# Performance work log

Hardware: AMD Instinct MI355X
Metric: run time of the kernel (lower is better)

Reference implementation:

```python
import jax, jax.numpy as jnp
import numpy as np
import math

B, S, HID = 2, 2048, 1024
NH = 16
HD = HID // NH  # 64
CHUNK = 128  # min(128, S) from the module


def setup_inputs() -> dict:
    key = jax.random.key(0)
    ks = jax.random.split(key, 8)
    scale = 1.0 / math.sqrt(HID)
    return {
        "hidden_states": jax.random.normal(ks[0], (B, S, HID), jnp.float32),
        "attention_mask": jnp.zeros((B, S, S), jnp.float32),
        "Wq": jax.random.normal(ks[1], (HID, HID), jnp.float32) * scale,
        "bq": jnp.zeros((HID,), jnp.float32),
        "Wk": jax.random.normal(ks[2], (HID, HID), jnp.float32) * scale,
        "bk": jnp.zeros((HID,), jnp.float32),
        "Wv": jax.random.normal(ks[3], (HID, HID), jnp.float32) * scale,
        "bv": jnp.zeros((HID,), jnp.float32),
        "head_weights": jnp.ones((NH,), jnp.float32),
    }


def _split_heads(x):
    # [B,S,HID] -> [B,NH,S,HD]
    b, s, _ = x.shape
    return x.reshape(b, s, NH, HD).transpose(0, 2, 1, 3)


def reference(hidden_states, attention_mask, Wq, bq, Wk, bk, Wv, bv, head_weights):
    # nn.Linear: y = x @ W.T + b
    q = _split_heads(hidden_states @ Wq.T + bq)  # [B,NH,S,HD]
    k = _split_heads(hidden_states @ Wk.T + bk)
    v = _split_heads(hidden_states @ Wv.T + bv)

    scores = jnp.einsum("bhqd,bhkd->bhqk", q, k) / math.sqrt(HD)
    scores = scores + attention_mask[:, None, :, :]  # additive mask broadcast over heads
    probs = jax.nn.softmax(scores, axis=-1)
    # dropout p=0.0 -> identity; post-softmax head-weight scaling (head_pruning)
    probs = probs * head_weights[None, :, None, None]
    ctx = jnp.einsum("bhqk,bhkd->bhqd", probs, v)  # [B,NH,S,HD]
    context_layer = ctx.transpose(0, 2, 1, 3).reshape(B, S, HID)

    # module returns the probs of the LAST query chunk of the python loop
    last_start = ((S + CHUNK - 1) // CHUNK - 1) * CHUNK
    output_attention_probs = probs[:, :, last_start:S, :]  # [B,NH,128,S]
    return context_layer, output_attention_probs
```

## Files before the change

### kernel.cpp

```cpp
#include <hip/hip_runtime.h>

typedef unsigned short u16;
typedef __attribute__((ext_vector_type(8))) short bf16x8;
typedef __attribute__((ext_vector_type(4))) float f32x4;

#define B_   2
#define S_   2048
#define HID_ 1024
#define NH_  16
#define HD_  64
#define SCALE_ 0.125f

__device__ __forceinline__ u16 f2bf(float f) {
    union { float f; unsigned int i; } v; v.f = f;
    unsigned int r = v.i + 0x7fffu + ((v.i >> 16) & 1u);
    return (u16)(r >> 16);
}
__device__ __forceinline__ bf16x8 ld8(const u16* p) {
    return *reinterpret_cast<const bf16x8*>(p);
}
__device__ __forceinline__ unsigned cvtpk(float lo, float hi) {
    unsigned r;
    asm("v_cvt_pk_bf16_f32 %0, %1, %2" : "=v"(r) : "v"(lo), "v"(hi));
    return r;
}
__device__ __forceinline__ void gll16(const u16* g, const u16* l) {
    __builtin_amdgcn_global_load_lds(
        (const __attribute__((address_space(1))) unsigned int*)g,
        (__attribute__((address_space(3))) unsigned int*)l, 16, 0, 0);
}

__global__ __launch_bounds__(256) void convert_bf16(
    const float* __restrict__ X, const float* __restrict__ W0,
    const float* __restrict__ W1, const float* __restrict__ W2,
    u16* __restrict__ Xb, u16* __restrict__ Wb)
{
    const size_t s = (size_t)blockIdx.x * 256 + threadIdx.x;
    const float* src; u16* dst; size_t off;
    if (s < 524288) { src = X; dst = Xb; off = s * 8; }
    else {
        const size_t t = s - 524288;
        const int w = (int)(t >> 17);
        off = (t & 131071) * 8;
        src = w == 0 ? W0 : w == 1 ? W1 : W2;
        dst = Wb + (size_t)w * 1048576;
    }
    f32x4 a = *(const f32x4*)(src + off);
    f32x4 b = *(const f32x4*)(src + off + 4);
    bf16x8 r;
    #pragma unroll
    for (int e = 0; e < 4; e++) { r[e] = (short)f2bf(a[e]); r[4 + e] = (short)f2bf(b[e]); }
    *(bf16x8*)(dst + off) = r;
}

__global__ __launch_bounds__(256) void mask_scan(
    const unsigned* __restrict__ m, unsigned* __restrict__ flag)
{
    const size_t i = ((size_t)blockIdx.x * 256 + threadIdx.x) * 8;
    const uint4* p = (const uint4*)(m + i);
    uint4 a = p[0], b = p[1];
    const unsigned M = 0x7fffffffu;
    unsigned v = (a.x & M) | (a.y & M) | (a.z & M) | (a.w & M)
               | (b.x & M) | (b.y & M) | (b.z & M) | (b.w & M);
    if (v) atomicOr(flag, 1u);
}

#define BK_ 32

__global__ __launch_bounds__(256) void qkv_mfma(
    const u16* __restrict__ Xb, const u16* __restrict__ Wb,
    const float* __restrict__ bq, const float* __restrict__ bk,
    const float* __restrict__ bv,
    u16* __restrict__ Q, u16* __restrict__ K, u16* __restrict__ V)
{
    __shared__ __align__(16) u16 As[128 * BK_];
    __shared__ __align__(16) u16 Bs[128 * BK_];

    const int tid  = threadIdx.x;
    const int wave = tid >> 6;
    const int lane = tid & 63;
    const int l16  = lane & 15;
    const int quad = lane >> 4;
    const int wr   = wave >> 1, wc = wave & 1;

    const int i0 = blockIdx.x * 128;
    const int j0 = blockIdx.y * 128;

    const int grow = (wave * 64 + lane) >> 2;
    const int gcol = (lane & 3) * 8;
    const u16* ldsA0 = As + wave * 512;
    const u16* ldsA1 = As + 2048 + wave * 512;
    const u16* ldsB0 = Bs + wave * 512;
    const u16* ldsB1 = Bs + 2048 + wave * 512;

    f32x4 acc[4][4] = {};

    for (int k0 = 0; k0 < HID_; k0 += BK_) {
        __syncthreads();
        gll16(Xb + (size_t)(i0 + grow) * HID_ + k0 + gcol, ldsA0);
        gll16(Xb + (size_t)(i0 + 64 + grow) * HID_ + k0 + gcol, ldsA1);
        gll16(Wb + (size_t)(j0 + grow) * HID_ + k0 + gcol, ldsB0);
        gll16(Wb + (size_t)(j0 + 64 + grow) * HID_ + k0 + gcol, ldsB1);
        __syncthreads();

        bf16x8 af[4], bfr[4];
        #pragma unroll
        for (int mt = 0; mt < 4; mt++)
            af[mt] = ld8(&As[(wr * 64 + mt * 16 + l16) * BK_ + quad * 8]);
        #pragma unroll
        for (int nt = 0; nt < 4; nt++)
            bfr[nt] = ld8(&Bs[(wc * 64 + nt * 16 + l16) * BK_ + quad * 8]);
        #pragma unroll
        for (int mt = 0; mt < 4; mt++)
            #pragma unroll
            for (int nt = 0; nt < 4; nt++)
                acc[mt][nt] = __builtin_amdgcn_mfma_f32_16x16x32_bf16(af[mt], bfr[nt], acc[mt][nt], 0, 0, 0);
    }

    const int which = j0 >> 10;
    const float* bias = which == 0 ? bq : which == 1 ? bk : bv;
    u16* Y            = which == 0 ? Q  : which == 1 ? K  : V;

    u16* bb = (wave < 2) ? (As + wave * 2048) : (Bs + (wave - 2) * 2048);

    #pragma unroll
    for (int p = 0; p < 2; p++) {
        __syncthreads();
        #pragma unroll
        for (int t2 = 0; t2 < 2; t2++) {
            const int nt = 2 * p + t2;
            const int j  = j0 + wc * 64 + nt * 16 + l16;
            const int jj = j & 1023;
            const float bv_ = bias[jj];
            #pragma unroll
            for (int mt = 0; mt < 4; mt++)
                #pragma unroll
                for (int r = 0; r < 4; r++) {
                    const int row = mt * 16 + quad * 4 + r;
                    const int col = t2 * 16 + l16;
                    const u16 val = f2bf(acc[mt][nt][r] + bv_);
                    if (which == 2)
                        bb[col * 64 + (row ^ ((col & 7) << 3))] = val;
                    else
                        bb[row * 32 + (col ^ ((row & 0xC) << 1))] = val;
                }
        }
        __syncthreads();
        #pragma unroll
        for (int k = 0; k < 4; k++) {
            const int c = lane + 64 * k;
            if (which == 2) {
                const int col  = c >> 3;
                const int row0 = (c & 7) * 8;
                bf16x8 v = ld8(&bb[col * 64 + (row0 ^ ((col & 7) << 3))]);
                const int j  = j0 + wc * 64 + p * 32 + col;
                const int jj = j & 1023;
                const int h = jj >> 6, d = jj & 63;
                const int i = i0 + wr * 64 + row0;
                const int b = i >> 11, s = i & (S_ - 1);
                *(bf16x8*)&Y[((size_t)(b * NH_ + h) * HD_ + d) * S_ + s] = v;
            } else {
                const int row  = c >> 2;
                const int col0 = (c & 3) * 8;
                bf16x8 v = ld8(&bb[row * 32 + (col0 ^ ((row & 0xC) << 1))]);
                const int j  = j0 + wc * 64 + p * 32 + col0;
                const int jj = j & 1023;
                const int h = jj >> 6, d = jj & 63;
                const int i = i0 + wr * 64 + row;
                const int b = i >> 11, s = i & (S_ - 1);
                *(bf16x8*)&Y[(((size_t)(b * NH_ + h) * S_ + s) * HD_) + d] = v;
            }
        }
    }
}

__global__ __launch_bounds__(256) void attn(
    const u16* __restrict__ Q, const u16* __restrict__ K, const u16* __restrict__ Vt,
    const float* __restrict__ mask, const float* __restrict__ hw,
    const unsigned* __restrict__ mflag,
    float* __restrict__ ctx, float* __restrict__ ml)
{
    __shared__ __align__(16) u16 Ks[2][64 * 64];
    __shared__ __align__(16) u16 Vs[2][64 * 64];
    __shared__ __align__(16) u16 Pl[4][16 * 64];

    const int usemask = (mflag[0] != 0);

    const int tid  = threadIdx.x;
    const int wave = tid >> 6;
    const int lane = tid & 63;
    const int l16  = lane & 15;
    const int quad = lane >> 4;
    const int x7   = l16 & 7;

    const int lin = blockIdx.x + 32 * (blockIdx.y + 16 * blockIdx.z);
    const int xcd = lin & 7, jj = lin >> 3;
    const int qb  = jj & 31;
    const int hb  = xcd * 4 + (jj >> 5);
    const int h   = hb & 15, b = hb >> 4;
    const int bh  = b * NH_ + h;

    const u16* Qh  = Q  + (size_t)bh * S_ * HD_;
    const u16* Kh  = K  + (size_t)bh * S_ * HD_;
    const u16* Vth = Vt + (size_t)bh * HD_ * S_;
    const float* Mb = mask + (size_t)b * S_ * S_;

    const int q0 = qb * 64 + wave * 16;

    bf16x8 qf0 = ld8(Qh + (size_t)(q0 + l16) * HD_ + quad * 8);
    bf16x8 qf1 = ld8(Qh + (size_t)(q0 + l16) * HD_ + 32 + quad * 8);

    f32x4 oacc[4] = {};
    float l_part[4] = {0.f, 0.f, 0.f, 0.f};

    const int srow = tid >> 3;
    const int sch  = tid & 7;
    const int ssw  = (sch ^ (srow & 7)) * 8;
    const int sL   = srow * 64 + ssw;

    {
        bf16x8 k0 = ld8(Kh + (size_t)srow * HD_ + sch * 8);
        bf16x8 k1 = ld8(Kh + (size_t)(srow + 32) * HD_ + sch * 8);
        bf16x8 v0 = ld8(Vth + (size_t)srow * S_ + sch * 8);
        bf16x8 v1 = ld8(Vth + (size_t)(srow + 32) * S_ + sch * 8);
        *(bf16x8*)&Ks[0][sL] = k0; *(bf16x8*)&Ks[0][sL + 2048] = k1;
        *(bf16x8*)&Vs[0][sL] = v0; *(bf16x8*)&Vs[0][sL + 2048] = v1;
    }
    __syncthreads();

    for (int t = 0; t < 32; ++t) {
        const int cur = t & 1;
        const int kt  = t * 64;
        const u16* Kb = Ks[cur];
        const u16* Vb = Vs[cur];

        bf16x8 kr0, kr1, vr0, vr1;
        if (t < 31) {
            const u16* Kg = Kh + (size_t)(kt + 64) * HD_;
            kr0 = ld8(Kg + (size_t)srow * HD_ + sch * 8);
            kr1 = ld8(Kg + (size_t)(srow + 32) * HD_ + sch * 8);
            vr0 = ld8(Vth + (size_t)srow * S_ + kt + 64 + sch * 8);
            vr1 = ld8(Vth + (size_t)(srow + 32) * S_ + kt + 64 + sch * 8);
        }

        f32x4 sacc[4] = {};
        __builtin_amdgcn_s_setprio(1);
        #pragma unroll
        for (int nb = 0; nb < 4; nb++) {
            const int base = (nb * 16 + l16) * 64;
            bf16x8 k0 = ld8(&Kb[base + ((quad ^ x7) * 8)]);
            bf16x8 k1 = ld8(&Kb[base + (((quad + 4) ^ x7) * 8)]);
            sacc[nb] = __builtin_amdgcn_mfma_f32_16x16x32_bf16(qf0, k0, sacc[nb], 0, 0, 0);
            sacc[nb] = __builtin_amdgcn_mfma_f32_16x16x32_bf16(qf1, k1, sacc[nb], 0, 0, 0);
        }
        __builtin_amdgcn_s_setprio(0);

        float p[4][4];
        if (usemask) {
            #pragma unroll
            for (int nb = 0; nb < 4; nb++)
                #pragma unroll
                for (int r = 0; r < 4; r++) {
                    const int qrow = q0 + quad * 4 + r;
                    const int key  = kt + nb * 16 + l16;
                    float s = sacc[nb][r] * SCALE_ + Mb[(size_t)qrow * S_ + key];
                    p[nb][r] = __expf(fminf(s, 80.f));
                    l_part[r] += p[nb][r];
                }
        } else {
            #pragma unroll
            for (int nb = 0; nb < 4; nb++)
                #pragma unroll
                for (int r = 0; r < 4; r++) {
                    p[nb][r] = __expf(fminf(sacc[nb][r] * SCALE_, 80.f));
                    l_part[r] += p[nb][r];
                }
        }

        {
            char* pbase = (char*)&Pl[wave][0];
            const int r0 = quad * 4;
            #pragma unroll
            for (int nb = 0; nb < 4; nb++) {
                const unsigned w01 = cvtpk(p[nb][0], p[nb][1]);
                const unsigned w23 = cvtpk(p[nb][2], p[nb][3]);
                const int c0 = nb * 32 + l16 * 2;
                *(u16*)(pbase + (r0 + 0) * 128 + (c0 ^ (((r0 + 0) & 7) << 4))) = (u16)w01;
                *(u16*)(pbase + (r0 + 1) * 128 + (c0 ^ (((r0 + 1) & 7) << 4))) = (u16)(w01 >> 16);
                *(u16*)(pbase + (r0 + 2) * 128 + (c0 ^ (((r0 + 2) & 7) << 4))) = (u16)w23;
                *(u16*)(pbase + (r0 + 3) * 128 + (c0 ^ (((r0 + 3) & 7) << 4))) = (u16)(w23 >> 16);
            }
        }

        __builtin_amdgcn_s_setprio(1);
        #pragma unroll
        for (int kb = 0; kb < 2; kb++) {
            const int c = kb * 4 + quad;
            bf16x8 pf = ld8(&Pl[wave][l16 * 64 + ((c ^ x7) * 8)]);
            #pragma unroll
            for (int db = 0; db < 4; db++) {
                bf16x8 vf = ld8(&Vb[(db * 16 + l16) * 64 + ((c ^ x7) * 8)]);
                oacc[db] = __builtin_amdgcn_mfma_f32_16x16x32_bf16(pf, vf, oacc[db], 0, 0, 0);
            }
        }
        __builtin_amdgcn_s_setprio(0);

        if (t < 31) {
            u16* Kd = Ks[cur ^ 1]; u16* Vd = Vs[cur ^ 1];
            *(bf16x8*)&Kd[sL] = kr0; *(bf16x8*)&Kd[sL + 2048] = kr1;
            *(bf16x8*)&Vd[sL] = vr0; *(bf16x8*)&Vd[sL + 2048] = vr1;
        }
        __syncthreads();
    }

    float l_i[4];
    #pragma unroll
    for (int r = 0; r < 4; r++) {
        float s = l_part[r];
        #pragma unroll
        for (int off = 1; off < 16; off <<= 1) s += __shfl_xor(s, off);
        l_i[r] = s;
    }

    const float hwf = hw[h];
    float invl[4];
    #pragma unroll
    for (int r = 0; r < 4; r++) invl[r] = hwf / l_i[r];

    #pragma unroll
    for (int db = 0; db < 4; db++)
        #pragma unroll
        for (int r = 0; r < 4; r++) {
            const int qrow = q0 + quad * 4 + r;
            ctx[((size_t)(b * S_ + qrow)) * HID_ + h * HD_ + db * 16 + l16] =
                oacc[db][r] * invl[r];
        }

    if (qb >= 30 && l16 == 0) {
        #pragma unroll
        for (int r = 0; r < 4; r++) {
            const int qrow = q0 + quad * 4 + r;
            ml[bh * 128 + (qrow - 1920)] = l_i[r];
        }
    }
}

__global__ __launch_bounds__(256) void probs_qk(
    const u16* __restrict__ Q, const u16* __restrict__ K,
    const float* __restrict__ mask, const float* __restrict__ hw,
    const unsigned* __restrict__ mflag, const float* __restrict__ ml,
    float* __restrict__ probs_out)
{
    const int usemask = (mflag[0] != 0);

    const int tid  = threadIdx.x;
    const int wave = tid >> 6;
    const int lane = tid & 63;
    const int l16  = lane & 15;
    const int quad = lane >> 4;

    const int rt = blockIdx.x & 1;
    const int ks = blockIdx.x >> 1;
    const int h  = blockIdx.y;
    const int b  = blockIdx.z;
    const int bh = b * NH_ + h;

    const u16* Qh = Q + (size_t)bh * S_ * HD_;
    const u16* Kh = K + (size_t)bh * S_ * HD_;
    const float* Mb = mask + (size_t)b * S_ * S_;

    const int q0 = 1920 + rt * 64 + wave * 16;

    bf16x8 qf0 = ld8(Qh + (size_t)(q0 + l16) * HD_ + quad * 8);
    bf16x8 qf1 = ld8(Qh + (size_t)(q0 + l16) * HD_ + 32 + quad * 8);

    const float hwf = hw[h];
    float invl[4];
    #pragma unroll
    for (int r = 0; r < 4; r++)
        invl[r] = hwf / ml[bh * 128 + (q0 - 1920) + quad * 4 + r];

    for (int kt = ks * 512; kt < ks * 512 + 512; kt += 64) {
        f32x4 sacc[4] = {};
        #pragma unroll
        for (int nb = 0; nb < 4; nb++) {
            const u16* krow = Kh + (size_t)(kt + nb * 16 + l16) * HD_ + quad * 8;
            bf16x8 k0 = ld8(krow);
            bf16x8 k1 = ld8(krow + 32);
            sacc[nb] = __builtin_amdgcn_mfma_f32_16x16x32_bf16(qf0, k0, sacc[nb], 0, 0, 0);
            sacc[nb] = __builtin_amdgcn_mfma_f32_16x16x32_bf16(qf1, k1, sacc[nb], 0, 0, 0);
        }
        #pragma unroll
        for (int nb = 0; nb < 4; nb++)
            #pragma unroll
            for (int r = 0; r < 4; r++) {
                const int qrow = q0 + quad * 4 + r;
                const int key  = kt + nb * 16 + l16;
                float s = sacc[nb][r] * SCALE_;
                if (usemask) s += Mb[(size_t)qrow * S_ + key];
                probs_out[((size_t)bh * 128 + (qrow - 1920)) * S_ + key] =
                    __expf(fminf(s, 80.f)) * invl[r];
            }
    }
}

extern "C" void kernel_launch(void* const* d_in, const int* in_sizes, int n_in,
                              void* d_out, int out_size, void* d_ws, size_t ws_size,
                              hipStream_t stream)
{
    const void* X = 0; const void* mask = 0; const void* hw = 0;
    const void* Wm[3] = {0, 0, 0}; const void* bm[3] = {0, 0, 0};
    int wi = 0, bi = 0;
    for (int i = 0; i < n_in; i++) {
        switch (in_sizes[i]) {
            case 4194304: X = d_in[i]; break;
            case 8388608: mask = d_in[i]; break;
            case 1048576: if (wi < 3) Wm[wi++] = d_in[i]; break;
            case 1024:    if (bi < 3) bm[bi++] = d_in[i]; break;
            case 16:      hw = d_in[i]; break;
            default: break;
        }
    }
    if (!X || !mask || wi != 3 || bi != 3 || !hw) {
        X = d_in[0]; mask = d_in[1];
        Wm[0] = d_in[2]; bm[0] = d_in[3];
        Wm[1] = d_in[4]; bm[1] = d_in[5];
        Wm[2] = d_in[6]; bm[2] = d_in[7];
        hw = d_in[8];
    }

    u16* Q  = (u16*)d_ws;
    u16* Kw = Q + 4194304ull;
    u16* Vw = Kw + 4194304ull;
    u16* Xb = Vw + 4194304ull;
    u16* Wb = Xb + 4194304ull;
    unsigned* flag = (unsigned*)(Wb + 3145728ull);
    float* ml = (float*)(flag + 64);

    float* ctx   = (float*)d_out;
    float* probs = ctx + (size_t)B_ * S_ * HID_;

    hipMemsetAsync(flag, 0, 4, stream);
    mask_scan<<<4096, 256, 0, stream>>>((const unsigned*)mask, flag);
    convert_bf16<<<3584, 256, 0, stream>>>(
        (const float*)X, (const float*)Wm[0], (const float*)Wm[1], (const float*)Wm[2],
        Xb, Wb);

    qkv_mfma<<<dim3(32, 24), dim3(256), 0, stream>>>(
        Xb, Wb, (const float*)bm[0], (const float*)bm[1], (const float*)bm[2],
        Q, Kw, Vw);

    attn<<<dim3(32, 16, 2), dim3(256), 0, stream>>>(
        Q, Kw, Vw, (const float*)mask, (const float*)hw, flag, ctx, ml);

    probs_qk<<<dim3(8, 16, 2), dim3(256), 0, stream>>>(
        Q, Kw, (const float*)mask, (const float*)hw, flag, ml, probs);
}
```

Measured before the change: 248.8 us.

## Fuse convert and mask-scan kernels, XCD-aware GEMM tiling, vectorized probs writes

```diff
diff --git a/kernel.cpp b/kernel.cpp
--- a/kernel.cpp
+++ b/kernel.cpp
@@ -30,39 +30,39 @@
         (__attribute__((address_space(3))) unsigned int*)l, 16, 0, 0);
 }
 
-__global__ __launch_bounds__(256) void convert_bf16(
+__global__ __launch_bounds__(256) void conv_scan(
     const float* __restrict__ X, const float* __restrict__ W0,
     const float* __restrict__ W1, const float* __restrict__ W2,
-    u16* __restrict__ Xb, u16* __restrict__ Wb)
+    const unsigned* __restrict__ m,
+    u16* __restrict__ Xb, u16* __restrict__ Wb, unsigned* __restrict__ flag)
 {
-    const size_t s = (size_t)blockIdx.x * 256 + threadIdx.x;
-    const float* src; u16* dst; size_t off;
-    if (s < 524288) { src = X; dst = Xb; off = s * 8; }
-    else {
-        const size_t t = s - 524288;
-        const int w = (int)(t >> 17);
-        off = (t & 131071) * 8;
-        src = w == 0 ? W0 : w == 1 ? W1 : W2;
-        dst = Wb + (size_t)w * 1048576;
-    }
-    f32x4 a = *(const f32x4*)(src + off);
-    f32x4 b = *(const f32x4*)(src + off + 4);
-    bf16x8 r;
-    #pragma unroll
-    for (int e = 0; e < 4; e++) { r[e] = (short)f2bf(a[e]); r[4 + e] = (short)f2bf(b[e]); }
-    *(bf16x8*)(dst + off) = r;
-}
-
-__global__ __launch_bounds__(256) void mask_scan(
-    const unsigned* __restrict__ m, unsigned* __restrict__ flag)
-{
-    const size_t i = ((size_t)blockIdx.x * 256 + threadIdx.x) * 8;
-    const uint4* p = (const uint4*)(m + i);
-    uint4 a = p[0], b = p[1];
-    const unsigned M = 0x7fffffffu;
-    unsigned v = (a.x & M) | (a.y & M) | (a.z & M) | (a.w & M)
-               | (b.x & M) | (b.y & M) | (b.z & M) | (b.w & M);
-    if (v) atomicOr(flag, 1u);
+    const int bx = blockIdx.x;
+    if (bx < 3584) {
+        const size_t s = (size_t)bx * 256 + threadIdx.x;
+        const float* src; u16* dst; size_t off;
+        if (s < 524288) { src = X; dst = Xb; off = s * 8; }
+        else {
+            const size_t t = s - 524288;
+            const int w = (int)(t >> 17);
+            off = (t & 131071) * 8;
+            src = w == 0 ? W0 : w == 1 ? W1 : W2;
+            dst = Wb + (size_t)w * 1048576;
+        }
+        f32x4 a = *(const f32x4*)(src + off);
+        f32x4 b = *(const f32x4*)(src + off + 4);
+        bf16x8 r;
+        #pragma unroll
+        for (int e = 0; e < 4; e++) { r[e] = (short)f2bf(a[e]); r[4 + e] = (short)f2bf(b[e]); }
+        *(bf16x8*)(dst + off) = r;
+    } else {
+        const size_t i = ((size_t)(bx - 3584) * 256 + threadIdx.x) * 8;
+        const uint4* p = (const uint4*)(m + i);
+        uint4 a = p[0], b = p[1];
+        const unsigned M = 0x7fffffffu;
+        unsigned v = (a.x & M) | (a.y & M) | (a.z & M) | (a.w & M)
+                   | (b.x & M) | (b.y & M) | (b.z & M) | (b.w & M);
+        if (v) atomicOr(flag, 1u);
+    }
 }
 
 #define BK_ 32
@@ -83,8 +83,11 @@
     const int quad = lane >> 4;
     const int wr   = wave >> 1, wc = wave & 1;
 
-    const int i0 = blockIdx.x * 128;
-    const int j0 = blockIdx.y * 128;
+    const int id  = blockIdx.x + 32 * blockIdx.y;
+    const int xcd = id & 7;
+    const int kk  = id >> 3;
+    const int i0  = (xcd * 4 + (kk & 3)) * 128;
+    const int j0  = (kk >> 2) * 128;
 
     const int grow = (wave * 64 + lane) >> 2;
     const int gcol = (lane & 3) * 8;
@@ -369,38 +372,44 @@
     const u16* Kh = K + (size_t)bh * S_ * HD_;
     const float* Mb = mask + (size_t)b * S_ * S_;
 
-    const int q0 = 1920 + rt * 64 + wave * 16;
-
-    bf16x8 qf0 = ld8(Qh + (size_t)(q0 + l16) * HD_ + quad * 8);
-    bf16x8 qf1 = ld8(Qh + (size_t)(q0 + l16) * HD_ + 32 + quad * 8);
-
-    const float hwf = hw[h];
-    float invl[4];
-    #pragma unroll
-    for (int r = 0; r < 4; r++)
-        invl[r] = hwf / ml[bh * 128 + (q0 - 1920) + quad * 4 + r];
-
-    for (int kt = ks * 512; kt < ks * 512 + 512; kt += 64) {
+    const int q0   = 1920 + rt * 64 + wave * 16;
+    const int qrow = q0 + l16;
+
+    bf16x8 qf0 = ld8(Qh + (size_t)qrow * HD_ + quad * 8);
+    bf16x8 qf1 = ld8(Qh + (size_t)qrow * HD_ + 32 + quad * 8);
+
+    const float invl = hw[h] / ml[bh * 128 + (qrow - 1920)];
+    float* Prow = probs_out + ((size_t)bh * 128 + (qrow - 1920)) * S_;
+    const float* Mrow = Mb + (size_t)qrow * S_;
+
+    for (int kt = ks * 256; kt < ks * 256 + 256; kt += 64) {
         f32x4 sacc[4] = {};
         #pragma unroll
         for (int nb = 0; nb < 4; nb++) {
             const u16* krow = Kh + (size_t)(kt + nb * 16 + l16) * HD_ + quad * 8;
-            bf16x8 k0 = ld8(krow);
-            bf16x8 k1 = ld8(krow + 32);
-            sacc[nb] = __builtin_amdgcn_mfma_f32_16x16x32_bf16(qf0, k0, sacc[nb], 0, 0, 0);
-            sacc[nb] = __builtin_amdgcn_mfma_f32_16x16x32_bf16(qf1, k1, sacc[nb], 0, 0, 0);
-        }
-        #pragma unroll
-        for (int nb = 0; nb < 4; nb++)
-            #pragma unroll
-            for (int r = 0; r < 4; r++) {
-                const int qrow = q0 + quad * 4 + r;
-                const int key  = kt + nb * 16 + l16;
-                float s = sacc[nb][r] * SCALE_;
-                if (usemask) s += Mb[(size_t)qrow * S_ + key];
-                probs_out[((size_t)bh * 128 + (qrow - 1920)) * S_ + key] =
-                    __expf(fminf(s, 80.f)) * invl[r];
+            bf16x8 kA0 = ld8(krow);
+            bf16x8 kA1 = ld8(krow + 32);
+            sacc[nb] = __builtin_amdgcn_mfma_f32_16x16x32_bf16(kA0, qf0, sacc[nb], 0, 0, 0);
+            sacc[nb] = __builtin_amdgcn_mfma_f32_16x16x32_bf16(kA1, qf1, sacc[nb], 0, 0, 0);
+        }
+        #pragma unroll
+        for (int nb = 0; nb < 4; nb++) {
+            const int kb0 = kt + nb * 16 + quad * 4;
+            float4 v;
+            if (usemask) {
+                const float4 mv = *(const float4*)&Mrow[kb0];
+                v.x = __expf(fminf(sacc[nb][0] * SCALE_ + mv.x, 80.f)) * invl;
+                v.y = __expf(fminf(sacc[nb][1] * SCALE_ + mv.y, 80.f)) * invl;
+                v.z = __expf(fminf(sacc[nb][2] * SCALE_ + mv.z, 80.f)) * invl;
+                v.w = __expf(fminf(sacc[nb][3] * SCALE_ + mv.w, 80.f)) * invl;
+            } else {
+                v.x = __expf(fminf(sacc[nb][0] * SCALE_, 80.f)) * invl;
+                v.y = __expf(fminf(sacc[nb][1] * SCALE_, 80.f)) * invl;
+                v.z = __expf(fminf(sacc[nb][2] * SCALE_, 80.f)) * invl;
+                v.w = __expf(fminf(sacc[nb][3] * SCALE_, 80.f)) * invl;
             }
+            *(float4*)&Prow[kb0] = v;
+        }
     }
 }
 
@@ -441,10 +450,9 @@
     float* probs = ctx + (size_t)B_ * S_ * HID_;
 
     hipMemsetAsync(flag, 0, 4, stream);
-    mask_scan<<<4096, 256, 0, stream>>>((const unsigned*)mask, flag);
-    convert_bf16<<<3584, 256, 0, stream>>>(
+    conv_scan<<<7680, 256, 0, stream>>>(
         (const float*)X, (const float*)Wm[0], (const float*)Wm[1], (const float*)Wm[2],
-        Xb, Wb);
+        (const unsigned*)mask, Xb, Wb, flag);
 
     qkv_mfma<<<dim3(32, 24), dim3(256), 0, stream>>>(
         Xb, Wb, (const float*)bm[0], (const float*)bm[1], (const float*)bm[2],
@@ -453,6 +461,6 @@
     attn<<<dim3(32, 16, 2), dim3(256), 0, stream>>>(
         Q, Kw, Vw, (const float*)mask, (const float*)hw, flag, ctx, ml);
 
-    probs_qk<<<dim3(8, 16, 2), dim3(256), 0, stream>>>(
+    probs_qk<<<dim3(16, 16, 2), dim3(256), 0, stream>>>(
         Q, Kw, (const float*)mask, (const float*)hw, flag, ml, probs);
 }
```

Measured after the change: 238.8 us. 4.0% less time.
